# Performance work log

Measured on AMD Instinct MI355X. Metric: run time of the kernel, lower is better.

## Reference

```python
import jax, jax.numpy as jnp
import numpy as np

V, H, B = 64, 128, 16384  # num_visible, num_hidden = alpha*V, batch of spin configs
ISCALE = 0.001


def setup_inputs() -> dict:
    key = jax.random.key(0)
    k1, k2, k3, k4 = jax.random.split(key, 4)
    x = jax.random.normal(k1, (B, V), dtype=jnp.float32)
    weight_1 = jax.random.normal(k2, (V, H), dtype=jnp.float32) * ISCALE
    weight_2 = jax.random.normal(k3, (H, V, V), dtype=jnp.float32) * (ISCALE / 10.0)
    hidden_bias = jax.random.normal(k4, (H,), dtype=jnp.float32) * ISCALE
    return {"x": x, "weight_1": weight_1, "weight_2": weight_2, "hidden_bias": hidden_bias}


def reference(x, weight_1, weight_2, hidden_bias):
    b, v = x.shape
    h = weight_2.shape[0]
    # order-1 term: (B,V) @ (V,H) -> (B,H)
    w1 = x @ weight_1
    # order-2 term: outer product of spins per sample, contracted with weight_2.
    # vis_ij: (B,V,V) flattened to (B,V*V); weight_2 flattened to (H,V*V) -> GEMM.
    vis_ij = jnp.einsum('mi,mj->mij', x, x).reshape(b, v * v)
    w2 = (vis_ij @ weight_2.reshape(h, v * v).T) * 0.5
    act = jnp.cos(hidden_bias + w1 + w2)  # (B,H)
    psi = jnp.prod(act, axis=-1)          # (B,)
    return psi
```

## Files before the change

### kernel.cpp

```cpp
#include <hip/hip_runtime.h>
#include <hip/hip_bf16.h>
#include <cstdint>

#define NV 64
#define NH 128
#define NB 16384
#define FRAG_ELEMS (130 * 8 * 512)

typedef __bf16 bf16x8_t __attribute__((ext_vector_type(8)));
typedef float f32x4_t __attribute__((ext_vector_type(4)));
typedef float f32x2_t __attribute__((ext_vector_type(2)));
typedef uint32_t u32x4_t __attribute__((ext_vector_type(4)));
typedef uint32_t u32x2_t __attribute__((ext_vector_type(2)));

__device__ __forceinline__ uint32_t bf16_rne(float f) {
  uint32_t u = __float_as_uint(f);
  return (u + 0x7fffu + ((u >> 16) & 1u)) >> 16;
}

__global__ void cvt_kernel(const float* __restrict__ w1f,
                           const float* __restrict__ w2f,
                           uint16_t* __restrict__ frag) {
  int tg = blockIdx.x * 256 + threadIdx.x;
  if (tg < 128 * 512) {
    int h = tg >> 9, k8 = tg & 511;
    const float* p = w2f + ((size_t)h << 12) + k8 * 8;
    float4 a = *(const float4*)p;
    float4 b = *(const float4*)(p + 4);
    uint4 o;
    o.x = (bf16_rne(0.5f * a.y) << 16) | bf16_rne(0.5f * a.x);
    o.y = (bf16_rne(0.5f * a.w) << 16) | bf16_rne(0.5f * a.z);
    o.z = (bf16_rne(0.5f * b.y) << 16) | bf16_rne(0.5f * b.x);
    o.w = (bf16_rne(0.5f * b.w) << 16) | bf16_rne(0.5f * b.z);
    int c2 = k8 >> 2, lhi = k8 & 3;
    int fh = h >> 4, l = lhi * 16 + (h & 15);
    *(uint4*)(frag + (((c2 * 8 + fh) * 64 + l) << 3)) = o;
  } else {
    int t2 = tg - 128 * 512;
    int h = t2 >> 3, j8 = t2 & 7;
    uint32_t v[8];
#pragma unroll
    for (int t = 0; t < 8; ++t)
      v[t] = bf16_rne(w1f[(j8 * 8 + t) * 128 + h]);
    int c2 = 128 + (j8 >> 2), lhi = j8 & 3;
    int fh = h >> 4, l = lhi * 16 + (h & 15);
    uint4 o;
    o.x = (v[1] << 16) | v[0];
    o.y = (v[3] << 16) | v[2];
    o.z = (v[5] << 16) | v[4];
    o.w = (v[7] << 16) | v[6];
    *(uint4*)(frag + (((c2 * 8 + fh) * 64 + l) << 3)) = o;
  }
}

__launch_bounds__(256, 2)
__global__ void rbm_kernel(const float* __restrict__ xg,
                           const float* __restrict__ biasg,
                           const __hip_bfloat16* __restrict__ frag,
                           float* __restrict__ outg) {
  __shared__ __align__(16) float xtile[64 * 68];
  __shared__ float part[4][64];

  const int tid  = threadIdx.x;
  const int hq   = tid >> 6;
  const int lane = tid & 63;
  const int c15  = lane & 15;
  const int q    = lane >> 4;
  const int mblk = blockIdx.x * 64;

  {
    int row = tid >> 2, seg = tid & 3;
    const float* p = xg + (size_t)(mblk + row) * NV + seg * 16;
    float4 v0 = *(const float4*)(p);
    float4 v1 = *(const float4*)(p + 4);
    float4 v2 = *(const float4*)(p + 8);
    float4 v3 = *(const float4*)(p + 12);
    float* d = &xtile[row * 68 + seg * 16];
    *(float4*)(d) = v0; *(float4*)(d + 4) = v1;
    *(float4*)(d + 8) = v2; *(float4*)(d + 12) = v3;
  }
  if (tid < 64) xtile[tid * 68 + 64] = 1.0f;
  __syncthreads();

  f32x2_t xf[4][2][4];
  const float* xrow[4];
#pragma unroll
  for (int im = 0; im < 4; ++im) {
    xrow[im] = &xtile[(im * 16 + c15) * 68];
#pragma unroll
    for (int jh = 0; jh < 2; ++jh) {
      float4 a = *(const float4*)(xrow[im] + jh * 32 + q * 8);
      float4 b = *(const float4*)(xrow[im] + jh * 32 + q * 8 + 4);
      xf[im][jh][0] = f32x2_t{a.x, a.y};
      xf[im][jh][1] = f32x2_t{a.z, a.w};
      xf[im][jh][2] = f32x2_t{b.x, b.y};
      xf[im][jh][3] = f32x2_t{b.z, b.w};
    }
  }

  const __hip_bfloat16* pb = frag + (size_t)(hq * 2) * 512 + lane * 8;
  bf16x8_t bnxt[2][2];
#pragma unroll
  for (int jh = 0; jh < 2; ++jh)
#pragma unroll
    for (int ih = 0; ih < 2; ++ih)
      bnxt[jh][ih] = *(const bf16x8_t*)(pb + jh * 4096 + ih * 512);

  f32x4_t acc[4][2];
#pragma unroll
  for (int im = 0; im < 4; ++im)
#pragma unroll
    for (int ih = 0; ih < 2; ++ih)
      acc[im][ih] = (f32x4_t)0.0f;

  float scur[4];
#pragma unroll
  for (int im = 0; im < 4; ++im) scur[im] = xrow[im][0];

  for (int c = 0; c < 65; ++c) {
    bf16x8_t bc[2][2];
#pragma unroll
    for (int jh = 0; jh < 2; ++jh)
#pragma unroll
      for (int ih = 0; ih < 2; ++ih)
        bc[jh][ih] = bnxt[jh][ih];
    pb += 8192;
    if (c < 64) {
#pragma unroll
      for (int jh = 0; jh < 2; ++jh)
#pragma unroll
        for (int ih = 0; ih < 2; ++ih)
          bnxt[jh][ih] = *(const bf16x8_t*)(pb + jh * 4096 + ih * 512);
    }
    float s[4];
#pragma unroll
    for (int im = 0; im < 4; ++im) s[im] = scur[im];
    if (c < 64) {
#pragma unroll
      for (int im = 0; im < 4; ++im) scur[im] = xrow[im][c + 1];
    }
#pragma unroll
    for (int jh = 0; jh < 2; ++jh) {
      bf16x8_t afrag[4];
#pragma unroll
      for (int im = 0; im < 4; ++im) {
        const f32x2_t s2 = f32x2_t{s[im], s[im]};
        u32x4_t adv;
#pragma unroll
        for (int t = 0; t < 4; ++t) {
          f32x2_t pr = s2 * xf[im][jh][t];
          u32x2_t u = __builtin_bit_cast(u32x2_t, pr);
          adv[t] = __builtin_amdgcn_perm(u[1], u[0], 0x07060302);
        }
        afrag[im] = __builtin_bit_cast(bf16x8_t, adv);
      }
#pragma unroll
      for (int ih = 0; ih < 2; ++ih)
#pragma unroll
        for (int im = 0; im < 4; ++im)
          acc[im][ih] = __builtin_amdgcn_mfma_f32_16x16x32_bf16(
              afrag[im], bc[jh][ih], acc[im][ih], 0, 0, 0);
    }
  }

  float bs[2];
#pragma unroll
  for (int ih = 0; ih < 2; ++ih)
    bs[ih] = biasg[hq * 32 + ih * 16 + c15];

  const float INV2PI = 0.15915494309189535f;
  float prod[4][4];
#pragma unroll
  for (int im = 0; im < 4; ++im)
#pragma unroll
    for (int r = 0; r < 4; ++r) {
      float c0 = __builtin_amdgcn_cosf((acc[im][0][r] + bs[0]) * INV2PI);
      float c1 = __builtin_amdgcn_cosf((acc[im][1][r] + bs[1]) * INV2PI);
      prod[im][r] = c0 * c1;
    }

#pragma unroll
  for (int ofs = 1; ofs < 16; ofs <<= 1)
#pragma unroll
    for (int im = 0; im < 4; ++im)
#pragma unroll
      for (int r = 0; r < 4; ++r)
        prod[im][r] *= __shfl_xor(prod[im][r], ofs, 16);

  if (c15 == 0) {
#pragma unroll
    for (int im = 0; im < 4; ++im)
#pragma unroll
      for (int r = 0; r < 4; ++r)
        part[hq][im * 16 + q * 4 + r] = prod[im][r];
  }
  __syncthreads();
  if (tid < 64) {
    float f = part[0][tid] * part[1][tid] * part[2][tid] * part[3][tid];
    outg[mblk + tid] = f;
  }
}

extern "C" void kernel_launch(void* const* d_in, const int* in_sizes, int n_in,
                              void* d_out, int out_size, void* d_ws, size_t ws_size,
                              hipStream_t stream) {
  const float* x   = (const float*)d_in[0];
  const float* w1f = (const float*)d_in[1];
  const float* w2f = (const float*)d_in[2];
  const float* hb  = (const float*)d_in[3];
  float* out = (float*)d_out;
  uint16_t* frag = (uint16_t*)d_ws;
  (void)in_sizes; (void)n_in; (void)out_size; (void)ws_size;

  cvt_kernel<<<(128 * 512 + 1024) / 256, 256, 0, stream>>>(w1f, w2f, frag);
  rbm_kernel<<<NB / 64, 256, 0, stream>>>(
      x, hb, (const __hip_bfloat16*)frag, out);
}
```

Before: 102.3 us.

## Exploit symmetry of x_i x_j to halve order-2 GEMM work

Because x_i x_j is symmetric, the weight conversion kernel now folds W[h,i,j] and W[h,j,i] into upper-triangular 8x8 blocks. That leaves 36 K-chunks (8 diagonal, 28 off-diagonal, plus one for the order-1 term) instead of 65. The main kernel walks only these chunks, cutting MFMA work and weight traffic roughly in half. The block also grows to 512 threads, with waves split over both sample rows and hidden columns, and the chunk loop is fully unrolled with compile-time block indices. This costs a more complex conversion kernel and higher register pressure from the unroll and the larger x register cache.

New measurement: 85.98 us. 1.19x faster.

```diff
diff --git a/kernel.cpp b/kernel.cpp
--- a/kernel.cpp
+++ b/kernel.cpp
@@ -5,7 +5,8 @@
 #define NV 64
 #define NH 128
 #define NB 16384
-#define FRAG_ELEMS (130 * 8 * 512)
+#define NCHUNK 37
+#define FRAG_ELEMS (NCHUNK * 8192)
 
 typedef __bf16 bf16x8_t __attribute__((ext_vector_type(8)));
 typedef float f32x4_t __attribute__((ext_vector_type(4)));
@@ -22,156 +23,176 @@
                            const float* __restrict__ w2f,
                            uint16_t* __restrict__ frag) {
   int tg = blockIdx.x * 256 + threadIdx.x;
-  if (tg < 128 * 512) {
-    int h = tg >> 9, k8 = tg & 511;
-    const float* p = w2f + ((size_t)h << 12) + k8 * 8;
-    float4 a = *(const float4*)p;
-    float4 b = *(const float4*)(p + 4);
-    uint4 o;
-    o.x = (bf16_rne(0.5f * a.y) << 16) | bf16_rne(0.5f * a.x);
-    o.y = (bf16_rne(0.5f * a.w) << 16) | bf16_rne(0.5f * a.z);
-    o.z = (bf16_rne(0.5f * b.y) << 16) | bf16_rne(0.5f * b.x);
-    o.w = (bf16_rne(0.5f * b.w) << 16) | bf16_rne(0.5f * b.z);
-    int c2 = k8 >> 2, lhi = k8 & 3;
-    int fh = h >> 4, l = lhi * 16 + (h & 15);
-    *(uint4*)(frag + (((c2 * 8 + fh) * 64 + l) << 3)) = o;
-  } else {
-    int t2 = tg - 128 * 512;
-    int h = t2 >> 3, j8 = t2 & 7;
-    uint32_t v[8];
-#pragma unroll
-    for (int t = 0; t < 8; ++t)
-      v[t] = bf16_rne(w1f[(j8 * 8 + t) * 128 + h]);
-    int c2 = 128 + (j8 >> 2), lhi = j8 & 3;
-    int fh = h >> 4, l = lhi * 16 + (h & 15);
-    uint4 o;
-    o.x = (v[1] << 16) | v[0];
-    o.y = (v[3] << 16) | v[2];
-    o.z = (v[5] << 16) | v[4];
-    o.w = (v[7] << 16) | v[6];
-    *(uint4*)(frag + (((c2 * 8 + fh) * 64 + l) << 3)) = o;
-  }
-}
-
-__launch_bounds__(256, 2)
+  int l = tg & 63, fh = (tg >> 6) & 7, c2 = tg >> 9;
+  int chunk = c2 >> 1, jh = c2 & 1;
+  int h = fh * 16 + (l & 15);
+  int kb = jh * 32 + (l >> 4) * 8;
+  uint32_t o16[8];
+#pragma unroll
+  for (int t = 0; t < 8; ++t) {
+    int slot = kb + t;
+    float v;
+    if (chunk < 8) {
+      int i = chunk * 8 + (slot >> 3), j = chunk * 8 + (slot & 7);
+      v = 0.5f * w2f[h * 4096 + i * 64 + j];
+    } else if (chunk < 36) {
+      int o = chunk - 8, I = 0;
+      while (o >= 7 - I) { o -= 7 - I; ++I; }
+      int J = I + 1 + o;
+      int i = I * 8 + (slot >> 3), j = J * 8 + (slot & 7);
+      v = 0.5f * (w2f[h * 4096 + i * 64 + j] + w2f[h * 4096 + j * 64 + i]);
+    } else {
+      v = w1f[slot * 128 + h];
+    }
+    o16[t] = bf16_rne(v);
+  }
+  uint4 o;
+  o.x = (o16[1] << 16) | o16[0];
+  o.y = (o16[3] << 16) | o16[2];
+  o.z = (o16[5] << 16) | o16[4];
+  o.w = (o16[7] << 16) | o16[6];
+  *(uint4*)(frag + ((size_t)(c2 * 8 + fh) << 9) + l * 8) = o;
+}
+
+__launch_bounds__(512, 2)
 __global__ void rbm_kernel(const float* __restrict__ xg,
                            const float* __restrict__ biasg,
                            const __hip_bfloat16* __restrict__ frag,
                            float* __restrict__ outg) {
-  __shared__ __align__(16) float xtile[64 * 68];
+  __shared__ __align__(16) float xtile[64 * 76];
   __shared__ float part[4][64];
 
   const int tid  = threadIdx.x;
-  const int hq   = tid >> 6;
+  const int wv   = tid >> 6;
+  const int wm   = wv & 1;
+  const int hq   = wv >> 1;
   const int lane = tid & 63;
   const int c15  = lane & 15;
   const int q    = lane >> 4;
   const int mblk = blockIdx.x * 64;
 
+  constexpr int CI[36] = {0,1,2,3,4,5,6,7, 0,0,0,0,0,0,0, 1,1,1,1,1,1,
+                          2,2,2,2,2, 3,3,3,3, 4,4,4, 5,5, 6};
+  constexpr int CJ[36] = {0,1,2,3,4,5,6,7, 1,2,3,4,5,6,7, 2,3,4,5,6,7,
+                          3,4,5,6,7, 4,5,6,7, 5,6,7, 6,7, 7};
+
   {
-    int row = tid >> 2, seg = tid & 3;
-    const float* p = xg + (size_t)(mblk + row) * NV + seg * 16;
-    float4 v0 = *(const float4*)(p);
-    float4 v1 = *(const float4*)(p + 4);
-    float4 v2 = *(const float4*)(p + 8);
-    float4 v3 = *(const float4*)(p + 12);
-    float* d = &xtile[row * 68 + seg * 16];
-    *(float4*)(d) = v0; *(float4*)(d + 4) = v1;
-    *(float4*)(d + 8) = v2; *(float4*)(d + 12) = v3;
-  }
-  if (tid < 64) xtile[tid * 68 + 64] = 1.0f;
+    int row = tid >> 3, grp = tid & 7;
+    const float* p = xg + (size_t)(mblk + row) * NV + grp * 8;
+    float4 a = *(const float4*)(p);
+    float4 b = *(const float4*)(p + 4);
+    *(float4*)(&xtile[row * 76 + grp * 8]) = a;
+    *(float4*)(&xtile[row * 76 + grp * 8 + 4]) = b;
+    xtile[row * 76 + 64 + grp] = 1.0f;
+  }
   __syncthreads();
 
-  f32x2_t xf[4][2][4];
-  const float* xrow[4];
-#pragma unroll
-  for (int im = 0; im < 4; ++im) {
-    xrow[im] = &xtile[(im * 16 + c15) * 68];
-#pragma unroll
-    for (int jh = 0; jh < 2; ++jh) {
-      float4 a = *(const float4*)(xrow[im] + jh * 32 + q * 8);
-      float4 b = *(const float4*)(xrow[im] + jh * 32 + q * 8 + 4);
-      xf[im][jh][0] = f32x2_t{a.x, a.y};
-      xf[im][jh][1] = f32x2_t{a.z, a.w};
-      xf[im][jh][2] = f32x2_t{b.x, b.y};
-      xf[im][jh][3] = f32x2_t{b.z, b.w};
-    }
-  }
-
-  const __hip_bfloat16* pb = frag + (size_t)(hq * 2) * 512 + lane * 8;
-  bf16x8_t bnxt[2][2];
-#pragma unroll
-  for (int jh = 0; jh < 2; ++jh)
-#pragma unroll
-    for (int ih = 0; ih < 2; ++ih)
-      bnxt[jh][ih] = *(const bf16x8_t*)(pb + jh * 4096 + ih * 512);
-
-  f32x4_t acc[4][2];
-#pragma unroll
-  for (int im = 0; im < 4; ++im)
+  const float* sx[2];
+  f32x2_t xb[2][32];
+#pragma unroll
+  for (int im = 0; im < 2; ++im) {
+    sx[im] = &xtile[(wm * 32 + im * 16 + c15) * 76];
+#pragma unroll
+    for (int g = 0; g < 8; ++g) {
+      float4 a = *(const float4*)(sx[im] + g * 8);
+      float4 b = *(const float4*)(sx[im] + g * 8 + 4);
+      xb[im][g * 4 + 0] = f32x2_t{a.x, a.y};
+      xb[im][g * 4 + 1] = f32x2_t{a.z, a.w};
+      xb[im][g * 4 + 2] = f32x2_t{b.x, b.y};
+      xb[im][g * 4 + 3] = f32x2_t{b.z, b.w};
+    }
+  }
+
+  const __hip_bfloat16* pw = frag + (size_t)hq * 1024 + lane * 8;
+
+  f32x4_t acc[2][2];
+#pragma unroll
+  for (int im = 0; im < 2; ++im)
 #pragma unroll
     for (int ih = 0; ih < 2; ++ih)
       acc[im][ih] = (f32x4_t)0.0f;
 
-  float scur[4];
-#pragma unroll
-  for (int im = 0; im < 4; ++im) scur[im] = xrow[im][0];
-
-  for (int c = 0; c < 65; ++c) {
+  bf16x8_t bn[2][2];
+#pragma unroll
+  for (int jh = 0; jh < 2; ++jh)
+#pragma unroll
+    for (int ih = 0; ih < 2; ++ih)
+      bn[jh][ih] = *(const bf16x8_t*)(pw + jh * 4096 + ih * 512);
+
+#pragma unroll
+  for (int c = 0; c < 36; ++c) {
     bf16x8_t bc[2][2];
 #pragma unroll
     for (int jh = 0; jh < 2; ++jh)
 #pragma unroll
       for (int ih = 0; ih < 2; ++ih)
-        bc[jh][ih] = bnxt[jh][ih];
-    pb += 8192;
-    if (c < 64) {
+        bc[jh][ih] = bn[jh][ih];
+    {
+      const __hip_bfloat16* pn = pw + (size_t)(c + 1) * 8192;
 #pragma unroll
       for (int jh = 0; jh < 2; ++jh)
 #pragma unroll
         for (int ih = 0; ih < 2; ++ih)
-          bnxt[jh][ih] = *(const bf16x8_t*)(pb + jh * 4096 + ih * 512);
-    }
-    float s[4];
-#pragma unroll
-    for (int im = 0; im < 4; ++im) s[im] = scur[im];
-    if (c < 64) {
-#pragma unroll
-      for (int im = 0; im < 4; ++im) scur[im] = xrow[im][c + 1];
-    }
+          bn[jh][ih] = *(const bf16x8_t*)(pn + jh * 4096 + ih * 512);
+    }
+    const int I = CI[c], J = CJ[c];
 #pragma unroll
     for (int jh = 0; jh < 2; ++jh) {
-      bf16x8_t afrag[4];
-#pragma unroll
-      for (int im = 0; im < 4; ++im) {
-        const f32x2_t s2 = f32x2_t{s[im], s[im]};
+      bf16x8_t afrag[2];
+#pragma unroll
+      for (int im = 0; im < 2; ++im) {
+        float s = sx[im][I * 8 + jh * 4 + q];
+        const f32x2_t s2 = f32x2_t{s, s};
         u32x4_t adv;
 #pragma unroll
-        for (int t = 0; t < 4; ++t) {
-          f32x2_t pr = s2 * xf[im][jh][t];
+        for (int tt = 0; tt < 4; ++tt) {
+          f32x2_t pr = s2 * xb[im][J * 4 + tt];
           u32x2_t u = __builtin_bit_cast(u32x2_t, pr);
-          adv[t] = __builtin_amdgcn_perm(u[1], u[0], 0x07060302);
+          adv[tt] = __builtin_amdgcn_perm(u[1], u[0], 0x07060302);
         }
         afrag[im] = __builtin_bit_cast(bf16x8_t, adv);
       }
 #pragma unroll
       for (int ih = 0; ih < 2; ++ih)
 #pragma unroll
-        for (int im = 0; im < 4; ++im)
+        for (int im = 0; im < 2; ++im)
           acc[im][ih] = __builtin_amdgcn_mfma_f32_16x16x32_bf16(
               afrag[im], bc[jh][ih], acc[im][ih], 0, 0, 0);
     }
   }
 
+#pragma unroll
+  for (int jh = 0; jh < 2; ++jh) {
+    bf16x8_t afrag[2];
+#pragma unroll
+    for (int im = 0; im < 2; ++im) {
+      float4 a = *(const float4*)(sx[im] + jh * 32 + q * 8);
+      float4 b = *(const float4*)(sx[im] + jh * 32 + q * 8 + 4);
+      const float pr[4][2] = {{a.x, a.y}, {a.z, a.w}, {b.x, b.y}, {b.z, b.w}};
+      u32x4_t adv;
+#pragma unroll
+      for (int tt = 0; tt < 4; ++tt)
+        adv[tt] = __builtin_amdgcn_perm(__float_as_uint(pr[tt][1]),
+                                        __float_as_uint(pr[tt][0]), 0x07060302);
+      afrag[im] = __builtin_bit_cast(bf16x8_t, adv);
+    }
+#pragma unroll
+    for (int ih = 0; ih < 2; ++ih)
+#pragma unroll
+      for (int im = 0; im < 2; ++im)
+        acc[im][ih] = __builtin_amdgcn_mfma_f32_16x16x32_bf16(
+            afrag[im], bn[jh][ih], acc[im][ih], 0, 0, 0);
+  }
+
   float bs[2];
 #pragma unroll
   for (int ih = 0; ih < 2; ++ih)
     bs[ih] = biasg[hq * 32 + ih * 16 + c15];
 
   const float INV2PI = 0.15915494309189535f;
-  float prod[4][4];
-#pragma unroll
-  for (int im = 0; im < 4; ++im)
+  float prod[2][4];
+#pragma unroll
+  for (int im = 0; im < 2; ++im)
 #pragma unroll
     for (int r = 0; r < 4; ++r) {
       float c0 = __builtin_amdgcn_cosf((acc[im][0][r] + bs[0]) * INV2PI);
@@ -182,17 +203,17 @@
 #pragma unroll
   for (int ofs = 1; ofs < 16; ofs <<= 1)
 #pragma unroll
-    for (int im = 0; im < 4; ++im)
+    for (int im = 0; im < 2; ++im)
 #pragma unroll
       for (int r = 0; r < 4; ++r)
         prod[im][r] *= __shfl_xor(prod[im][r], ofs, 16);
 
   if (c15 == 0) {
 #pragma unroll
-    for (int im = 0; im < 4; ++im)
+    for (int im = 0; im < 2; ++im)
 #pragma unroll
       for (int r = 0; r < 4; ++r)
-        part[hq][im * 16 + q * 4 + r] = prod[im][r];
+        part[hq][wm * 32 + im * 16 + q * 4 + r] = prod[im][r];
   }
   __syncthreads();
   if (tid < 64) {
@@ -212,7 +233,7 @@
   uint16_t* frag = (uint16_t*)d_ws;
   (void)in_sizes; (void)n_in; (void)out_size; (void)ws_size;
 
-  cvt_kernel<<<(128 * 512 + 1024) / 256, 256, 0, stream>>>(w1f, w2f, frag);
-  rbm_kernel<<<NB / 64, 256, 0, stream>>>(
+  cvt_kernel<<<148, 256, 0, stream>>>(w1f, w2f, frag);
+  rbm_kernel<<<NB / 64, 512, 0, stream>>>(
       x, hb, (const __hip_bfloat16*)frag, out);
 }
```
